# Kernel tuning notes

Measured on AMD Instinct MI355X. Metric: run time of the kernel, lower is better.

Reference implementation:

```python
import jax, jax.numpy as jnp
import numpy as np

KNOW, ITEM, D, L, LAT, B, S = 1024, 20000, 128, 2, 256, 256, 200
NTOT = ITEM + KNOW
E1, E2 = 32768, 160000


def graph_layer(h, W, a, src, dst, n):
    # GAT-style: gather src/dst, edge MLP, segment softmax over dst, weighted scatter-sum
    z = h @ W                                              # [N, D]
    e = jax.nn.leaky_relu((jnp.concatenate([z[src], z[dst]], axis=-1) @ a)[:, 0])  # [E]
    m = jax.ops.segment_max(e, dst, num_segments=n)
    m = jnp.where(jnp.isfinite(m), m, 0.0)                 # nodes with no in-edges
    w = jnp.exp(e - m[dst])                                # [E]
    den = jax.ops.segment_sum(w, dst, num_segments=n)      # [N]
    num = jax.ops.segment_sum(w[:, None] * z[src], dst, num_segments=n)  # [N, D]
    return jnp.where(den[:, None] > 0, num / jnp.maximum(den, 1e-12)[:, None], 0.0)


def setup_inputs() -> dict:
    key = jax.random.key(0)
    ks = jax.random.split(key, 32)
    p = lambda i, shp: jax.random.normal(ks[i], shp, dtype=jnp.float32) * 0.05
    inp = {
        'p_rec': jax.random.randint(ks[0], (B, S), 0, ITEM),
        'p_target': jax.random.randint(ks[1], (B,), 0, S),
        'a_rec': jax.random.randint(ks[2], (B, S), 0, 3),
        'kn_rec': jax.random.uniform(ks[3], (B, S, KNOW), dtype=jnp.float32),
        'kn_num': jnp.ones((B, S), dtype=jnp.float32),
        'src1': jax.random.randint(ks[4], (E1,), 0, KNOW),
        'dst1': jax.random.randint(ks[5], (E1,), 0, KNOW),
        'src2': jax.random.randint(ks[6], (E2,), 0, NTOT),
        'dst2': jax.random.randint(ks[7], (E2,), 0, NTOT),
        'src3': jax.random.randint(ks[8], (E2,), 0, NTOT),
        'dst3': jax.random.randint(ks[9], (E2,), 0, NTOT),
        'kn_table': p(10, (KNOW, D)),
        'exer_table': p(11, (ITEM, D)),
        'ans_table': p(12, (3, D)),
        'gW': p(13, (L, 3, D, D)),
        'gA': p(14, (L, 3, 2 * D, 1)),
        'raW1': p(15, (L, D, D)),
        'raB1': jnp.zeros((L, D), jnp.float32),
        'raW2': p(16, (L, D, 1)),
        'actW1': p(17, (3 * D, LAT)),
        'actB1': jnp.zeros((LAT,), jnp.float32),
        'actW2': p(18, (LAT, ITEM)),
        'actB2': jnp.zeros((ITEM,), jnp.float32),
        'vW1': p(19, (3, 3 * D, LAT)),
        'vB1': jnp.zeros((3, LAT), jnp.float32),
        'vW2': p(20, (3, LAT, 1)),
        'vB2': jnp.zeros((3, 1), jnp.float32),
    }
    return inp


def reference(p_rec, p_target, a_rec, kn_rec, kn_num, src1, dst1, src2, dst2, src3, dst3,
              kn_table, exer_table, ans_table, gW, gA, raW1, raB1, raW2,
              actW1, actB1, actW2, actB2, vW1, vB1, vW2, vB2):
    kn, ex = kn_table, exer_table
    for l in range(L):  # GraphEncoder: stacked Fusion blocks (distinct params)
        k_dir = graph_layer(kn, gW[l, 0], gA[l, 0], src1, dst1, KNOW)
        ek = jnp.concatenate([ex, kn], axis=0)             # [NTOT, D]
        kfe = graph_layer(ek, gW[l, 1], gA[l, 1], src2, dst2, NTOT)
        efk = graph_layer(ek, gW[l, 2], gA[l, 2], src3, dst3, NTOT)
        A_, B_ = k_dir, kfe[ITEM:]
        ra = lambda x: jnp.tanh(x @ raW1[l] + raB1[l]) @ raW2[l]  # [KNOW, 1]
        s = jax.nn.softmax(jnp.concatenate([ra(A_), ra(B_)], axis=1), axis=1)
        kn = s[:, :1] * A_ + s[:, 1:2] * B_
        ex = efk[:ITEM]
    # hidden_layer
    be = ex[p_rec]                                         # [B, S, D]
    ba = ans_table[a_rec]                                  # [B, S, D]
    bk = jnp.einsum('bsk,kd->bsd', kn_rec, kn) / kn_num[..., None]
    item = jnp.concatenate([be, ba, bk], axis=-1)          # [B, S, 3D]
    m = (jnp.arange(S)[None, :] < (p_target + 1)[:, None]).astype(item.dtype)
    h = (item * m[..., None]).sum(axis=1) / m.sum(axis=1, keepdims=True)  # [B, 3D]
    logits = jnp.tanh(h @ actW1 + actB1) @ actW2 + actB2   # [B, ITEM]
    vh = jnp.tanh(jnp.einsum('bd,kdl->kbl', h, vW1) + vB1[:, None, :])
    vals = jnp.einsum('kbl,klo->kbo', vh, vW2) + vB2[:, None, :]  # [3, B, 1]
    return logits, vals[0], vals[1], vals[2]
```

## Files before the change

### kernel.cpp

```cpp
#include <hip/hip_runtime.h>

#define D 128
#define KNOW 1024
#define ITEM 20000
#define NTOT (ITEM + KNOW)
#define LAYERS 2
#define LAT 256
#define BB 256
#define SS 200
#define H3 (3 * D)
#define CH 4
#define ZROWS 64
#define NBK (KNOW / ZROWS)
#define NBN ((NTOT + ZROWS - 1) / ZROWS)
#define XPITCH 68

__global__ __launch_bounds__(256) void zdv(
    const float* __restrict__ Xe, const float* __restrict__ Xk,
    const float* __restrict__ gW, const float* __restrict__ gA, int layer,
    float* __restrict__ z1, float* __restrict__ z2, float* __restrict__ z3,
    float* __restrict__ ds1, float* __restrict__ dd1,
    float* __restrict__ ds2, float* __restrict__ dd2,
    float* __restrict__ ds3, float* __restrict__ dd3)
{
    __shared__ __align__(16) float xT[D * XPITCH];
    int bid = blockIdx.x;
    int g, row0, nmax;
    if (bid < NBK)            { g = 0; row0 = bid * ZROWS;                nmax = KNOW; }
    else if (bid < NBK + NBN) { g = 1; row0 = (bid - NBK) * ZROWS;        nmax = NTOT; }
    else                      { g = 2; row0 = (bid - NBK - NBN) * ZROWS;  nmax = NTOT; }
    const float* W = gW + (size_t)(layer * 3 + g) * D * D;
    const float* A = gA + (size_t)(layer * 3 + g) * 2 * D;
    float* Z  = (g == 0) ? z1  : (g == 1 ? z2  : z3);
    float* DS = (g == 0) ? ds1 : (g == 1 ? ds2 : ds3);
    float* DD = (g == 0) ? dd1 : (g == 1 ? dd2 : dd3);

    int tid = threadIdx.x;
#pragma unroll
    for (int i = 0; i < 8; ++i) {
        int flat = tid + i * 256;
        int row  = flat >> 5;
        int f4   = flat & 31;
        int grow = row0 + row;
        float4 v = make_float4(0.f, 0.f, 0.f, 0.f);
        if (grow < nmax) {
            const float* src = (g == 0) ? (Xk + (size_t)grow * D)
                             : (grow < ITEM ? Xe + (size_t)grow * D
                                            : Xk + (size_t)(grow - ITEM) * D);
            v = *(const float4*)(src + f4 * 4);
        }
        int slot = row ^ ((f4 & 7) << 2);
        int kk = f4 * 4;
        xT[(kk + 0) * XPITCH + slot] = v.x;
        xT[(kk + 1) * XPITCH + slot] = v.y;
        xT[(kk + 2) * XPITCH + slot] = v.z;
        xT[(kk + 3) * XPITCH + slot] = v.w;
    }
    __syncthreads();

    int cg = tid & 31;
    int rg = tid >> 5;
    int c0 = cg * 4;
    int r0a = rg * 8, r0b = rg * 8 + 4;

    float acc[8][4];
#pragma unroll
    for (int r = 0; r < 8; ++r)
#pragma unroll
        for (int c = 0; c < 4; ++c) acc[r][c] = 0.f;

#pragma unroll 4
    for (int k = 0; k < D; ++k) {
        float4 wv = *(const float4*)(W + (size_t)k * D + c0);
        int xc = ((k >> 2) & 7) << 2;
        float4 xa = *(const float4*)&xT[k * XPITCH + (r0a ^ xc)];
        float4 xb = *(const float4*)&xT[k * XPITCH + (r0b ^ xc)];
        acc[0][0] = fmaf(xa.x, wv.x, acc[0][0]); acc[0][1] = fmaf(xa.x, wv.y, acc[0][1]);
        acc[0][2] = fmaf(xa.x, wv.z, acc[0][2]); acc[0][3] = fmaf(xa.x, wv.w, acc[0][3]);
        acc[1][0] = fmaf(xa.y, wv.x, acc[1][0]); acc[1][1] = fmaf(xa.y, wv.y, acc[1][1]);
        acc[1][2] = fmaf(xa.y, wv.z, acc[1][2]); acc[1][3] = fmaf(xa.y, wv.w, acc[1][3]);
        acc[2][0] = fmaf(xa.z, wv.x, acc[2][0]); acc[2][1] = fmaf(xa.z, wv.y, acc[2][1]);
        acc[2][2] = fmaf(xa.z, wv.z, acc[2][2]); acc[2][3] = fmaf(xa.z, wv.w, acc[2][3]);
        acc[3][0] = fmaf(xa.w, wv.x, acc[3][0]); acc[3][1] = fmaf(xa.w, wv.y, acc[3][1]);
        acc[3][2] = fmaf(xa.w, wv.z, acc[3][2]); acc[3][3] = fmaf(xa.w, wv.w, acc[3][3]);
        acc[4][0] = fmaf(xb.x, wv.x, acc[4][0]); acc[4][1] = fmaf(xb.x, wv.y, acc[4][1]);
        acc[4][2] = fmaf(xb.x, wv.z, acc[4][2]); acc[4][3] = fmaf(xb.x, wv.w, acc[4][3]);
        acc[5][0] = fmaf(xb.y, wv.x, acc[5][0]); acc[5][1] = fmaf(xb.y, wv.y, acc[5][1]);
        acc[5][2] = fmaf(xb.y, wv.z, acc[5][2]); acc[5][3] = fmaf(xb.y, wv.w, acc[5][3]);
        acc[6][0] = fmaf(xb.z, wv.x, acc[6][0]); acc[6][1] = fmaf(xb.z, wv.y, acc[6][1]);
        acc[6][2] = fmaf(xb.z, wv.z, acc[6][2]); acc[6][3] = fmaf(xb.z, wv.w, acc[6][3]);
        acc[7][0] = fmaf(xb.w, wv.x, acc[7][0]); acc[7][1] = fmaf(xb.w, wv.y, acc[7][1]);
        acc[7][2] = fmaf(xb.w, wv.z, acc[7][2]); acc[7][3] = fmaf(xb.w, wv.w, acc[7][3]);
    }

#pragma unroll
    for (int r = 0; r < 8; ++r) {
        int grow = row0 + ((r < 4) ? (r0a + r) : (r0b + r - 4));
        if (grow < nmax) {
            float4 v = make_float4(acc[r][0], acc[r][1], acc[r][2], acc[r][3]);
            *(float4*)(Z + (size_t)grow * D + c0) = v;
        }
    }

    float4 as = *(const float4*)(A + c0);
    float4 ad = *(const float4*)(A + D + c0);
    float ps[8], pd[8];
#pragma unroll
    for (int r = 0; r < 8; ++r) {
        ps[r] = acc[r][0] * as.x + acc[r][1] * as.y + acc[r][2] * as.z + acc[r][3] * as.w;
        pd[r] = acc[r][0] * ad.x + acc[r][1] * ad.y + acc[r][2] * ad.z + acc[r][3] * ad.w;
    }
#pragma unroll
    for (int m = 16; m; m >>= 1) {
#pragma unroll
        for (int r = 0; r < 8; ++r) {
            ps[r] += __shfl_xor(ps[r], m, 64);
            pd[r] += __shfl_xor(pd[r], m, 64);
        }
    }
    if (cg == 0) {
#pragma unroll
        for (int r = 0; r < 8; ++r) {
            int grow = row0 + ((r < 4) ? (r0a + r) : (r0b + r - 4));
            if (grow < nmax) { DS[grow] = ps[r]; DD[grow] = pd[r]; }
        }
    }
}

__global__ void hist3(const int* __restrict__ d1, const int* __restrict__ d2, const int* __restrict__ d3,
                      int E1, int E2, int* __restrict__ c1, int* __restrict__ c2, int* __restrict__ c3) {
    int i = blockIdx.x * blockDim.x + threadIdx.x;
    if (i < E1) atomicAdd(&c1[d1[i]], 1);
    else if (i < E1 + E2) { int d = d2[i - E1]; if (d >= ITEM) atomicAdd(&c2[d - ITEM], 1); }
    else if (i < E1 + 2 * E2) atomicAdd(&c3[d3[i - E1 - E2]], 1);
}

__global__ __launch_bounds__(1024) void exscan3(int* __restrict__ c1, int* __restrict__ o1,
                                                int* __restrict__ c2, int* __restrict__ o2,
                                                int* __restrict__ c3, int* __restrict__ o3) {
    int g = blockIdx.x;
    int* cnt = (g == 0) ? c1 : (g == 1 ? c2 : c3);
    int* off = (g == 0) ? o1 : (g == 1 ? o2 : o3);
    int n = (g == 2) ? NTOT : KNOW;
    __shared__ int wsum[16];
    __shared__ int carry;
    int tid = threadIdx.x, lane = tid & 63, wid = tid >> 6;
    if (tid == 0) { carry = 0; off[0] = 0; }
    __syncthreads();
    for (int base = 0; base < n; base += 1024) {
        int i = base + tid;
        int v = (i < n) ? cnt[i] : 0;
        int x = v;
#pragma unroll
        for (int d = 1; d < 64; d <<= 1) { int t = __shfl_up(x, d, 64); x += (lane >= d) ? t : 0; }
        if (lane == 63) wsum[wid] = x;
        __syncthreads();
        if (wid == 0) {
            int w = (lane < 16) ? wsum[lane] : 0;
#pragma unroll
            for (int d = 1; d < 16; d <<= 1) { int t = __shfl_up(w, d, 64); w += (lane >= d) ? t : 0; }
            if (lane < 16) wsum[lane] = w;
        }
        __syncthreads();
        int incl = x + ((wid > 0) ? wsum[wid - 1] : 0) + carry;
        if (i < n) { off[i + 1] = incl; cnt[i] = incl - v; }
        __syncthreads();
        if (tid == 1023) carry = incl;
        __syncthreads();
    }
}

__global__ void scatter3(const int* __restrict__ s1, const int* __restrict__ d1,
                         const int* __restrict__ s2, const int* __restrict__ d2,
                         const int* __restrict__ s3, const int* __restrict__ d3,
                         int E1, int E2, int* __restrict__ cur1, int* __restrict__ cur2, int* __restrict__ cur3,
                         int* __restrict__ e1, int* __restrict__ e2, int* __restrict__ e3) {
    int i = blockIdx.x * blockDim.x + threadIdx.x;
    if (i < E1) { int p = atomicAdd(&cur1[d1[i]], 1); e1[p] = s1[i]; }
    else if (i < E1 + E2) { int j = i - E1; int d = d2[j]; if (d >= ITEM) { int p = atomicAdd(&cur2[d - ITEM], 1); e2[p] = s2[j]; } }
    else if (i < E1 + 2 * E2) { int j = i - E1 - E2; int p = atomicAdd(&cur3[d3[j]], 1); e3[p] = s3[j]; }
}

__device__ __forceinline__ void agg_row(const float* __restrict__ Z, const float* __restrict__ dsrc,
                                        float dd, const int* __restrict__ es, int e0, int e1,
                                        int lane, float* __restrict__ acc) {
#pragma unroll
    for (int q = 0; q < 8; ++q) acc[q] = 0.f;
    if (e1 <= e0) return;
    float mx = -3.4e38f;
    for (int e = e0 + lane; e < e1; e += 64) {
        float t = dsrc[es[e]] + dd;
        t = (t > 0.f) ? t : 0.01f * t;
        mx = fmaxf(mx, t);
    }
#pragma unroll
    for (int o = 32; o; o >>= 1) mx = fmaxf(mx, __shfl_xor(mx, o, 64));
    int eg = lane >> 4, cs = lane & 15;
    float den = 0.f;
    for (int e = e0 + eg; e < e1; e += 4) {
        int s = es[e];
        float t = dsrc[s] + dd;
        t = (t > 0.f) ? t : 0.01f * t;
        float w = __expf(t - mx);
        den += w;
        const float4* zr = (const float4*)(Z + (size_t)s * D + cs * 8);
        float4 za = zr[0], zb = zr[1];
        acc[0] = fmaf(w, za.x, acc[0]); acc[1] = fmaf(w, za.y, acc[1]);
        acc[2] = fmaf(w, za.z, acc[2]); acc[3] = fmaf(w, za.w, acc[3]);
        acc[4] = fmaf(w, zb.x, acc[4]); acc[5] = fmaf(w, zb.y, acc[5]);
        acc[6] = fmaf(w, zb.z, acc[6]); acc[7] = fmaf(w, zb.w, acc[7]);
    }
#pragma unroll
    for (int m = 16; m <= 32; m <<= 1) {
        den += __shfl_xor(den, m, 64);
#pragma unroll
        for (int q = 0; q < 8; ++q) acc[q] += __shfl_xor(acc[q], m, 64);
    }
    float inv = 1.f / fmaxf(den, 1e-12f);
#pragma unroll
    for (int q = 0; q < 8; ++q) acc[q] *= inv;
}

__global__ __launch_bounds__(256) void agg3c(
    const float* __restrict__ z1, const float* __restrict__ z2, const float* __restrict__ z3,
    const float* __restrict__ ds1, const float* __restrict__ dd1,
    const float* __restrict__ ds2, const float* __restrict__ dd2,
    const float* __restrict__ ds3, const float* __restrict__ dd3,
    const int* __restrict__ off1, const int* __restrict__ es1,
    const int* __restrict__ off2, const int* __restrict__ es2,
    const int* __restrict__ off3, const int* __restrict__ es3,
    const float* __restrict__ raW1, const float* __restrict__ raB1,
    const float* __restrict__ raW2, float* __restrict__ buf)
{
    int wv = threadIdx.x >> 6, lane = threadIdx.x & 63;
    int eg = lane >> 4, cs = lane & 15;
    if (blockIdx.x < KNOW / 4) {
        __shared__ float ABs[4][2][D];
        int i = blockIdx.x * 4 + wv;
        float accA[8], accB[8];
        agg_row(z1, ds1, dd1[i], es1, off1[i], off1[i + 1], lane, accA);
        agg_row(z2, ds2, dd2[ITEM + i], es2, off2[i], off2[i + 1], lane, accB);
        if (eg == 0) {
            *(float4*)&ABs[wv][0][cs * 8]     = make_float4(accA[0], accA[1], accA[2], accA[3]);
            *(float4*)&ABs[wv][0][cs * 8 + 4] = make_float4(accA[4], accA[5], accA[6], accA[7]);
            *(float4*)&ABs[wv][1][cs * 8]     = make_float4(accB[0], accB[1], accB[2], accB[3]);
            *(float4*)&ABs[wv][1][cs * 8 + 4] = make_float4(accB[4], accB[5], accB[6], accB[7]);
        }
        __syncthreads();
        int j0 = lane * 2;
        float b0 = raB1[j0], b1 = raB1[j0 + 1];
        float aA0 = b0, aA1 = b1, aB0 = b0, aB1 = b1;
#pragma unroll 4
        for (int k = 0; k < D; ++k) {
            float av = ABs[wv][0][k], bv = ABs[wv][1][k];
            float2 w = *(const float2*)(raW1 + (size_t)k * D + j0);
            aA0 = fmaf(av, w.x, aA0); aA1 = fmaf(av, w.y, aA1);
            aB0 = fmaf(bv, w.x, aB0); aB1 = fmaf(bv, w.y, aB1);
        }
        float2 w2 = *(const float2*)(raW2 + j0);
        float pA = tanhf(aA0) * w2.x + tanhf(aA1) * w2.y;
        float pB = tanhf(aB0) * w2.x + tanhf(aB1) * w2.y;
#pragma unroll
        for (int o = 32; o; o >>= 1) { pA += __shfl_xor(pA, o, 64); pB += __shfl_xor(pB, o, 64); }
        float mx2 = fmaxf(pA, pB);
        float eA = __expf(pA - mx2), eB = __expf(pB - mx2);
        float s = 1.f / (eA + eB);
        float sA = eA * s, sB = eB * s;
        float2 Av = *(float2*)&ABs[wv][0][j0];
        float2 Bv = *(float2*)&ABs[wv][1][j0];
        *(float2*)(buf + (size_t)(ITEM + i) * D + j0) =
            make_float2(sA * Av.x + sB * Bv.x, sA * Av.y + sB * Bv.y);
    } else {
        int row = (blockIdx.x - KNOW / 4) * 4 + wv;
        if (row < ITEM) {
            float acc[8];
            agg_row(z3, ds3, dd3[row], es3, off3[row], off3[row + 1], lane, acc);
            if (eg == 0) {
                *(float4*)(buf + (size_t)row * D + cs * 8)     = make_float4(acc[0], acc[1], acc[2], acc[3]);
                *(float4*)(buf + (size_t)row * D + cs * 8 + 4) = make_float4(acc[4], acc[5], acc[6], acc[7]);
            }
        }
    }
}

__global__ __launch_bounds__(256) void krowk(const float* __restrict__ kn_rec, const float* __restrict__ kn_num,
                                             const int* __restrict__ p_target, float* __restrict__ krowP) {
    int b = blockIdx.x, ch = blockIdx.y;
    int cnt = p_target[b] + 1;
    int per = (SS + CH - 1) / CH;
    int s0 = ch * per, s1 = s0 + per;
    if (s1 > cnt) s1 = cnt;
    int k0 = threadIdx.x * 4;
    float4 a = make_float4(0.f, 0.f, 0.f, 0.f);
    for (int s = s0; s < s1; ++s) {
        float inv = 1.f / kn_num[b * SS + s];
        float4 v = *(const float4*)(kn_rec + ((size_t)b * SS + s) * KNOW + k0);
        a.x += v.x * inv; a.y += v.y * inv; a.z += v.z * inv; a.w += v.w * inv;
    }
    *(float4*)(krowP + ((size_t)ch * BB + b) * KNOW + k0) = a;
}

__global__ __launch_bounds__(512) void hker(const float* __restrict__ ex, const float* __restrict__ ans_table,
                                            const int* __restrict__ p_rec, const int* __restrict__ a_rec,
                                            const int* __restrict__ p_target, const float* __restrict__ krowP,
                                            const float* __restrict__ kn, float* __restrict__ h) {
    int b = blockIdx.x;
    int j = threadIdx.x & 127, sg = threadIdx.x >> 7;
    int cnt = p_target[b] + 1;
    __shared__ int pidx[SS], aidx[SS];
    __shared__ float kr[KNOW];
    __shared__ float red[4][3][128];
    for (int i = threadIdx.x; i < cnt; i += 512) { pidx[i] = p_rec[b * SS + i]; aidx[i] = a_rec[b * SS + i]; }
    for (int i = threadIdx.x; i < KNOW; i += 512) {
        float s = 0.f;
#pragma unroll
        for (int c = 0; c < CH; ++c) s += krowP[((size_t)c * BB + b) * KNOW + i];
        kr[i] = s;
    }
    __syncthreads();
    float accE = 0.f, accA = 0.f;
    for (int s = sg; s < cnt; s += 4) {
        accE += ex[(size_t)pidx[s] * D + j];
        accA += ans_table[aidx[s] * D + j];
    }
    float accK = 0.f;
    for (int k = sg * 256; k < sg * 256 + 256; ++k) accK += kr[k] * kn[(size_t)k * D + j];
    red[sg][0][j] = accE; red[sg][1][j] = accA; red[sg][2][j] = accK;
    __syncthreads();
    if (sg == 0) {
        float inv = 1.f / (float)cnt;
        float e = (red[0][0][j] + red[1][0][j] + red[2][0][j] + red[3][0][j]) * inv;
        float a = (red[0][1][j] + red[1][1][j] + red[2][1][j] + red[3][1][j]) * inv;
        float kv = (red[0][2][j] + red[1][2][j] + red[2][2][j] + red[3][2][j]) * inv;
        h[b * H3 + j] = e;
        h[b * H3 + D + j] = a;
        h[b * H3 + 2 * D + j] = kv;
    }
}

__global__ __launch_bounds__(256) void hidden_gemm(const float* __restrict__ h,
                                                   const float* __restrict__ actW1, const float* __restrict__ actB1,
                                                   const float* __restrict__ vW1, const float* __restrict__ vB1,
                                                   float* __restrict__ hid) {
    __shared__ float hT[H3 * 17];
    int tid = threadIdx.x;
    int b0 = blockIdx.y * 16;
    for (int idx = tid; idx < 16 * H3; idx += 256) {
        int r = idx / H3, k = idx - r * H3;
        hT[k * 17 + r] = h[(size_t)(b0 + r) * H3 + k];
    }
    __syncthreads();
    int j = blockIdx.x * 64 + (tid & 63);
    int head = j >> 8, jj = j & 255;
    int rg = tid >> 6, r0 = rg * 4;
    const float* W = (head == 0) ? actW1 : (vW1 + (size_t)(head - 1) * H3 * LAT);
    float bias = (head == 0) ? actB1[jj] : vB1[(head - 1) * LAT + jj];
    float acc[4] = {bias, bias, bias, bias};
#pragma unroll 4
    for (int k = 0; k < H3; ++k) {
        float w = W[(size_t)k * LAT + jj];
        float h0 = hT[k * 17 + r0 + 0];
        float h1 = hT[k * 17 + r0 + 1];
        float h2 = hT[k * 17 + r0 + 2];
        float h3 = hT[k * 17 + r0 + 3];
        acc[0] = fmaf(h0, w, acc[0]);
        acc[1] = fmaf(h1, w, acc[1]);
        acc[2] = fmaf(h2, w, acc[2]);
        acc[3] = fmaf(h3, w, acc[3]);
    }
#pragma unroll
    for (int r = 0; r < 4; ++r)
        hid[((size_t)head * BB + (b0 + r0 + r)) * LAT + jj] = tanhf(acc[r]);
}

__global__ __launch_bounds__(256) void logitsker(const float* __restrict__ hid, const float* __restrict__ actW2,
                                                 const float* __restrict__ actB2, float* __restrict__ out) {
    __shared__ float hT[LAT * 33];
    int tid = threadIdx.x;
    int b0 = blockIdx.y * 32;
    for (int idx = tid; idx < 32 * LAT; idx += 256) {
        int r = idx >> 8, k = idx & 255;
        hT[k * 33 + r] = hid[(size_t)(b0 + r) * LAT + k];
    }
    __syncthreads();
    int lane6 = tid & 63;
    int rg = tid >> 6, r0 = rg * 8;
    int ibase = blockIdx.x * 256 + lane6;
    int icol[4], icl[4];
    float bias[4];
#pragma unroll
    for (int c = 0; c < 4; ++c) {
        icol[c] = ibase + c * 64;
        icl[c] = icol[c] < ITEM ? icol[c] : (ITEM - 1);
        bias[c] = actB2[icl[c]];
    }
    float acc[8][4];
#pragma unroll
    for (int r = 0; r < 8; ++r)
#pragma unroll
        for (int c = 0; c < 4; ++c) acc[r][c] = bias[c];
#pragma unroll 2
    for (int k = 0; k < LAT; ++k) {
        float w0 = actW2[(size_t)k * ITEM + icl[0]];
        float w1 = actW2[(size_t)k * ITEM + icl[1]];
        float w2 = actW2[(size_t)k * ITEM + icl[2]];
        float w3 = actW2[(size_t)k * ITEM + icl[3]];
        const float* hp = &hT[k * 33 + r0];
#pragma unroll
        for (int r = 0; r < 8; ++r) {
            float hv = hp[r];
            acc[r][0] = fmaf(hv, w0, acc[r][0]);
            acc[r][1] = fmaf(hv, w1, acc[r][1]);
            acc[r][2] = fmaf(hv, w2, acc[r][2]);
            acc[r][3] = fmaf(hv, w3, acc[r][3]);
        }
    }
#pragma unroll
    for (int c = 0; c < 4; ++c) {
        if (icol[c] < ITEM) {
#pragma unroll
            for (int r = 0; r < 8; ++r)
                out[(size_t)(b0 + r0 + r) * ITEM + icol[c]] = acc[r][c];
        }
    }
}

__global__ __launch_bounds__(256) void valsker(const float* __restrict__ hid, const float* __restrict__ vW2,
                                               const float* __restrict__ vB2, float* __restrict__ out) {
    int idx = blockIdx.x * 4 + (threadIdx.x >> 6);
    int lane = threadIdx.x & 63;
    if (idx >= 3 * BB) return;
    int k = idx / BB, b = idx - k * BB;
    const float* vh = hid + ((size_t)(k + 1) * BB + b) * LAT;
    float4 a = ((const float4*)vh)[lane];
    float4 w = ((const float4*)(vW2 + k * LAT))[lane];
    float s = a.x * w.x + a.y * w.y + a.z * w.z + a.w * w.w;
#pragma unroll
    for (int o = 32; o; o >>= 1) s += __shfl_down(s, o, 64);
    if (lane == 0) out[(size_t)BB * ITEM + k * BB + b] = s + vB2[k];
}

extern "C" void kernel_launch(void* const* d_in, const int* in_sizes, int n_in,
                              void* d_out, int out_size, void* d_ws, size_t ws_size,
                              hipStream_t stream) {
    const int*   p_rec      = (const int*)d_in[0];
    const int*   p_target   = (const int*)d_in[1];
    const int*   a_rec      = (const int*)d_in[2];
    const float* kn_rec     = (const float*)d_in[3];
    const float* kn_num     = (const float*)d_in[4];
    const int*   src1       = (const int*)d_in[5];
    const int*   dst1       = (const int*)d_in[6];
    const int*   src2       = (const int*)d_in[7];
    const int*   dst2       = (const int*)d_in[8];
    const int*   src3       = (const int*)d_in[9];
    const int*   dst3       = (const int*)d_in[10];
    const float* kn_table   = (const float*)d_in[11];
    const float* exer_table = (const float*)d_in[12];
    const float* ans_table  = (const float*)d_in[13];
    const float* gW         = (const float*)d_in[14];
    const float* gA         = (const float*)d_in[15];
    const float* raW1       = (const float*)d_in[16];
    const float* raB1       = (const float*)d_in[17];
    const float* raW2       = (const float*)d_in[18];
    const float* actW1      = (const float*)d_in[19];
    const float* actB1      = (const float*)d_in[20];
    const float* actW2      = (const float*)d_in[21];
    const float* actB2      = (const float*)d_in[22];
    const float* vW1        = (const float*)d_in[23];
    const float* vB1        = (const float*)d_in[24];
    const float* vW2        = (const float*)d_in[25];
    const float* vB2        = (const float*)d_in[26];
    const int E1 = in_sizes[5], E2 = in_sizes[7];

    float* base = (float*)d_ws;
    size_t o = 0;
    auto alloc = [&](size_t n) -> float* { float* p = base + o; o += (n + 3) & ~(size_t)3; return p; };
    float* buf  = alloc((size_t)NTOT * D);
    float* z1   = alloc((size_t)KNOW * D);
    float* z2   = alloc((size_t)NTOT * D);
    float* z3   = alloc((size_t)NTOT * D);
    float* ds1 = alloc(KNOW);  float* dd1 = alloc(KNOW);
    float* ds2 = alloc(NTOT);  float* dd2 = alloc(NTOT);
    float* ds3 = alloc(NTOT);  float* dd3 = alloc(NTOT);
    int* cnts = (int*)alloc(2 * KNOW + NTOT);
    int* cnt1 = cnts, *cnt2 = cnts + KNOW, *cnt3 = cnts + 2 * KNOW;
    int* off1 = (int*)alloc(KNOW + 1);
    int* off2 = (int*)alloc(KNOW + 1);
    int* off3 = (int*)alloc(NTOT + 1);
    int* es1  = (int*)alloc(E1);
    int* es2  = (int*)alloc(E2);
    int* es3  = (int*)alloc(E2);
    float* krowP = alloc((size_t)CH * BB * KNOW);
    float* hbuf  = alloc((size_t)BB * H3);
    float* hid   = alloc((size_t)4 * BB * LAT);

    hipMemsetAsync(cnts, 0, sizeof(int) * (2 * KNOW + NTOT), stream);

    int etot = E1 + 2 * E2;
    hist3<<<(etot + 255) / 256, 256, 0, stream>>>(dst1, dst2, dst3, E1, E2, cnt1, cnt2, cnt3);
    exscan3<<<3, 1024, 0, stream>>>(cnt1, off1, cnt2, off2, cnt3, off3);
    scatter3<<<(etot + 255) / 256, 256, 0, stream>>>(src1, dst1, src2, dst2, src3, dst3,
                                                     E1, E2, cnt1, cnt2, cnt3, es1, es2, es3);

    int aggBlocks = KNOW / 4 + ITEM / 4;
    for (int l = 0; l < LAYERS; ++l) {
        const float* Xe = (l == 0) ? exer_table : buf;
        const float* Xk = (l == 0) ? kn_table : (buf + (size_t)ITEM * D);
        zdv<<<NBK + 2 * NBN, 256, 0, stream>>>(Xe, Xk, gW, gA, l, z1, z2, z3,
                                               ds1, dd1, ds2, dd2, ds3, dd3);
        agg3c<<<aggBlocks, 256, 0, stream>>>(z1, z2, z3, ds1, dd1, ds2, dd2, ds3, dd3,
                                             off1, es1, off2, es2, off3, es3,
                                             raW1 + (size_t)l * D * D, raB1 + (size_t)l * D,
                                             raW2 + (size_t)l * D, buf);
    }

    krowk<<<dim3(BB, CH), 256, 0, stream>>>(kn_rec, kn_num, p_target, krowP);
    hker<<<BB, 512, 0, stream>>>(buf, ans_table, p_rec, a_rec, p_target, krowP, buf + (size_t)ITEM * D, hbuf);
    hidden_gemm<<<dim3(16, 16), 256, 0, stream>>>(hbuf, actW1, actB1, vW1, vB1, hid);
    logitsker<<<dim3((ITEM + 255) / 256, 8), 256, 0, stream>>>(hid, actW2, actB2, (float*)d_out);
    valsker<<<(3 * BB + 3) / 4, 256, 0, stream>>>(hid, vW2, vB2, (float*)d_out);
}
```

Before: 301.6 us.

## Fuse kn_rec reduction into hker, trim efk CSR to item rows, serialize scan

Removes the separate krowk kernel and its krowP partial buffer: hker now reads kn_rec directly per batch row with float2 loads and accumulates the knowledge weights itself, cutting a launch and a global round trip but giving each batch only one block for that streaming pass. The efk graph CSR now histograms and scatters only edges whose destination is an item row, since only those rows are consumed. The exclusive scan is rewritten to give each thread a contiguous chunk with a single block-wide scan instead of a multi-pass loop with several barriers.

```diff
diff --git a/kernel.cpp b/kernel.cpp
--- a/kernel.cpp
+++ b/kernel.cpp
@@ -9,7 +9,6 @@
 #define BB 256
 #define SS 200
 #define H3 (3 * D)
-#define CH 4
 #define ZROWS 64
 #define NBK (KNOW / ZROWS)
 #define NBN ((NTOT + ZROWS - 1) / ZROWS)
@@ -132,7 +131,7 @@
     int i = blockIdx.x * blockDim.x + threadIdx.x;
     if (i < E1) atomicAdd(&c1[d1[i]], 1);
     else if (i < E1 + E2) { int d = d2[i - E1]; if (d >= ITEM) atomicAdd(&c2[d - ITEM], 1); }
-    else if (i < E1 + 2 * E2) atomicAdd(&c3[d3[i - E1 - E2]], 1);
+    else if (i < E1 + 2 * E2) { int d = d3[i - E1 - E2]; if (d < ITEM) atomicAdd(&c3[d], 1); }
 }
 
 __global__ __launch_bounds__(1024) void exscan3(int* __restrict__ c1, int* __restrict__ o1,
@@ -141,32 +140,38 @@
     int g = blockIdx.x;
     int* cnt = (g == 0) ? c1 : (g == 1 ? c2 : c3);
     int* off = (g == 0) ? o1 : (g == 1 ? o2 : o3);
-    int n = (g == 2) ? NTOT : KNOW;
-    __shared__ int wsum[16];
-    __shared__ int carry;
+    int n = (g == 2) ? ITEM : KNOW;
     int tid = threadIdx.x, lane = tid & 63, wid = tid >> 6;
-    if (tid == 0) { carry = 0; off[0] = 0; }
-    __syncthreads();
-    for (int base = 0; base < n; base += 1024) {
-        int i = base + tid;
-        int v = (i < n) ? cnt[i] : 0;
-        int x = v;
-#pragma unroll
-        for (int d = 1; d < 64; d <<= 1) { int t = __shfl_up(x, d, 64); x += (lane >= d) ? t : 0; }
-        if (lane == 63) wsum[wid] = x;
-        __syncthreads();
-        if (wid == 0) {
-            int w = (lane < 16) ? wsum[lane] : 0;
-#pragma unroll
-            for (int d = 1; d < 16; d <<= 1) { int t = __shfl_up(w, d, 64); w += (lane >= d) ? t : 0; }
-            if (lane < 16) wsum[lane] = w;
-        }
-        __syncthreads();
-        int incl = x + ((wid > 0) ? wsum[wid - 1] : 0) + carry;
-        if (i < n) { off[i + 1] = incl; cnt[i] = incl - v; }
-        __syncthreads();
-        if (tid == 1023) carry = incl;
-        __syncthreads();
+    int L = (n + 1023) >> 10;
+    int i0 = tid * L;
+    int sum = 0;
+    for (int q = 0; q < L; ++q) {
+        int i = i0 + q;
+        if (i < n) sum += cnt[i];
+    }
+    int x = sum;
+#pragma unroll
+    for (int d = 1; d < 64; d <<= 1) { int t = __shfl_up(x, d, 64); if (lane >= d) x += t; }
+    __shared__ int ws[16];
+    if (lane == 63) ws[wid] = x;
+    __syncthreads();
+    if (wid == 0) {
+        int w = (lane < 16) ? ws[lane] : 0;
+#pragma unroll
+        for (int d = 1; d < 16; d <<= 1) { int t = __shfl_up(w, d, 64); if (lane >= d) w += t; }
+        if (lane < 16) ws[lane] = w;
+    }
+    __syncthreads();
+    int run = x - sum + ((wid > 0) ? ws[wid - 1] : 0);
+    if (tid == 0) off[0] = 0;
+    for (int q = 0; q < L; ++q) {
+        int i = i0 + q;
+        if (i < n) {
+            int v = cnt[i];
+            cnt[i] = run;
+            run += v;
+            off[i + 1] = run;
+        }
     }
 }
 
@@ -178,7 +183,7 @@
     int i = blockIdx.x * blockDim.x + threadIdx.x;
     if (i < E1) { int p = atomicAdd(&cur1[d1[i]], 1); e1[p] = s1[i]; }
     else if (i < E1 + E2) { int j = i - E1; int d = d2[j]; if (d >= ITEM) { int p = atomicAdd(&cur2[d - ITEM], 1); e2[p] = s2[j]; } }
-    else if (i < E1 + 2 * E2) { int j = i - E1 - E2; int p = atomicAdd(&cur3[d3[j]], 1); e3[p] = s3[j]; }
+    else if (i < E1 + 2 * E2) { int j = i - E1 - E2; int d = d3[j]; if (d < ITEM) { int p = atomicAdd(&cur3[d], 1); e3[p] = s3[j]; } }
 }
 
 __device__ __forceinline__ void agg_row(const float* __restrict__ Z, const float* __restrict__ dsrc,
@@ -283,39 +288,30 @@
     }
 }
 
-__global__ __launch_bounds__(256) void krowk(const float* __restrict__ kn_rec, const float* __restrict__ kn_num,
-                                             const int* __restrict__ p_target, float* __restrict__ krowP) {
-    int b = blockIdx.x, ch = blockIdx.y;
-    int cnt = p_target[b] + 1;
-    int per = (SS + CH - 1) / CH;
-    int s0 = ch * per, s1 = s0 + per;
-    if (s1 > cnt) s1 = cnt;
-    int k0 = threadIdx.x * 4;
-    float4 a = make_float4(0.f, 0.f, 0.f, 0.f);
-    for (int s = s0; s < s1; ++s) {
-        float inv = 1.f / kn_num[b * SS + s];
-        float4 v = *(const float4*)(kn_rec + ((size_t)b * SS + s) * KNOW + k0);
-        a.x += v.x * inv; a.y += v.y * inv; a.z += v.z * inv; a.w += v.w * inv;
-    }
-    *(float4*)(krowP + ((size_t)ch * BB + b) * KNOW + k0) = a;
-}
-
 __global__ __launch_bounds__(512) void hker(const float* __restrict__ ex, const float* __restrict__ ans_table,
                                             const int* __restrict__ p_rec, const int* __restrict__ a_rec,
-                                            const int* __restrict__ p_target, const float* __restrict__ krowP,
+                                            const int* __restrict__ p_target,
+                                            const float* __restrict__ kn_rec, const float* __restrict__ kn_num,
                                             const float* __restrict__ kn, float* __restrict__ h) {
     int b = blockIdx.x;
-    int j = threadIdx.x & 127, sg = threadIdx.x >> 7;
+    int tid = threadIdx.x;
+    int j = tid & 127, sg = tid >> 7;
     int cnt = p_target[b] + 1;
     __shared__ int pidx[SS], aidx[SS];
     __shared__ float kr[KNOW];
     __shared__ float red[4][3][128];
-    for (int i = threadIdx.x; i < cnt; i += 512) { pidx[i] = p_rec[b * SS + i]; aidx[i] = a_rec[b * SS + i]; }
-    for (int i = threadIdx.x; i < KNOW; i += 512) {
-        float s = 0.f;
-#pragma unroll
-        for (int c = 0; c < CH; ++c) s += krowP[((size_t)c * BB + b) * KNOW + i];
-        kr[i] = s;
+    for (int i = tid; i < cnt; i += 512) { pidx[i] = p_rec[b * SS + i]; aidx[i] = a_rec[b * SS + i]; }
+    {
+        float a0 = 0.f, a1 = 0.f;
+        const float* kb = kn_rec + (size_t)b * SS * KNOW + tid * 2;
+        const float* nb = kn_num + (size_t)b * SS;
+#pragma unroll 2
+        for (int s = 0; s < cnt; ++s) {
+            float inv = 1.f / nb[s];
+            float2 v = *(const float2*)(kb + (size_t)s * KNOW);
+            a0 = fmaf(v.x, inv, a0); a1 = fmaf(v.y, inv, a1);
+        }
+        kr[tid * 2] = a0; kr[tid * 2 + 1] = a1;
     }
     __syncthreads();
     float accE = 0.f, accA = 0.f;
@@ -486,11 +482,10 @@
     int* cnt1 = cnts, *cnt2 = cnts + KNOW, *cnt3 = cnts + 2 * KNOW;
     int* off1 = (int*)alloc(KNOW + 1);
     int* off2 = (int*)alloc(KNOW + 1);
-    int* off3 = (int*)alloc(NTOT + 1);
+    int* off3 = (int*)alloc(ITEM + 1);
     int* es1  = (int*)alloc(E1);
     int* es2  = (int*)alloc(E2);
     int* es3  = (int*)alloc(E2);
-    float* krowP = alloc((size_t)CH * BB * KNOW);
     float* hbuf  = alloc((size_t)BB * H3);
     float* hid   = alloc((size_t)4 * BB * LAT);
 
@@ -514,8 +509,8 @@
                                              raW2 + (size_t)l * D, buf);
     }
 
-    krowk<<<dim3(BB, CH), 256, 0, stream>>>(kn_rec, kn_num, p_target, krowP);
-    hker<<<BB, 512, 0, stream>>>(buf, ans_table, p_rec, a_rec, p_target, krowP, buf + (size_t)ITEM * D, hbuf);
+    hker<<<BB, 512, 0, stream>>>(buf, ans_table, p_rec, a_rec, p_target, kn_rec, kn_num,
+                                 buf + (size_t)ITEM * D, hbuf);
     hidden_gemm<<<dim3(16, 16), 256, 0, stream>>>(hbuf, actW1, actB1, vW1, vB1, hid);
     logitsker<<<dim3((ITEM + 255) / 256, 8), 256, 0, stream>>>(hid, actW2, actB2, (float*)d_out);
     valsker<<<(3 * BB + 3) / 4, 256, 0, stream>>>(hid, vW2, vB2, (float*)d_out);
```

After: 320.9 us. 6.4% more time.
